# Kernel optimization log

Measured on AMD Instinct MI355X. Metric: run time of the kernel, lower is better.

Reference implementation:

```python
import jax, jax.numpy as jnp
import numpy as np

TEMPERATURE = 0.1
EPS = 1e-8


def setup_inputs() -> dict:
    key = jax.random.key(0)
    k1, k2 = jax.random.split(key)
    N, D = 4096, 512
    features = jax.random.normal(k1, (N, D), dtype=jnp.float32)
    labels = jax.random.randint(k2, (N,), 0, 100, dtype=jnp.int64)
    return {"features": features, "labels": labels}


def reference(features, labels):
    # FFT along feature dim -> complex (N, D)
    cf = jnp.fft.fft(features)
    N = cf.shape[0]

    # All-pairs complex dot product expressed as a GEMM:
    # Re(sum_d u_d * conj(v_d)) for every (anchor, contrast) pair -> (N, N)
    dot_real = jnp.real(cf @ jnp.conj(cf).T)

    # L2 norm of complex vectors: sqrt(sum |cf|^2) -> (N,)
    norms = jnp.linalg.norm(cf, axis=-1)

    sim = dot_real / (norms[:, None] * norms[None, :])  # cosine sim (N, N)
    sim = sim / TEMPERATURE

    # Positive-pair mask (same label), excluding the diagonal (self)
    same_label = (labels[:, None] == labels[None, :]).astype(sim.dtype)
    logits_mask = 1.0 - jnp.eye(N, dtype=sim.dtype)
    mask = same_label * logits_mask

    # Faithful to the original: exp without max-subtraction (sim bounded by 1/tau)
    exp_logits = jnp.exp(sim) * logits_mask
    log_prob = sim - jnp.log(exp_logits.sum(axis=1, keepdims=True))

    mean_log_prob_pos = (mask * log_prob).sum(axis=1) / (mask.sum(axis=1) + EPS)
    return -mean_log_prob_pos.mean()
```

## Files before the change

### kernel.cpp

```cpp
#include <hip/hip_runtime.h>
#include <hip/hip_bf16.h>
#include <math.h>


#define NROWS 4096
#define DDIM  512
#define TW    64
#define NBG   (NROWS / TW)
#define NTRI  (NBG * (NBG + 1) / 2)
#define NGRP  (NROWS / 16)
#define NSTEP (DDIM / 32)

typedef __attribute__((ext_vector_type(8))) short  short8;
typedef __attribute__((ext_vector_type(4))) float  floatx4;

__device__ inline unsigned short f2bf(float x) {
    unsigned u = __float_as_uint(x);
    return (unsigned short)((u + 0x7FFFu + ((u >> 16) & 1u)) >> 16);
}

__device__ inline float dpp_add16(float v) {
    v += __int_as_float(__builtin_amdgcn_update_dpp(
        0, __float_as_int(v), 0xB1, 0xF, 0xF, true));
    v += __int_as_float(__builtin_amdgcn_update_dpp(
        0, __float_as_int(v), 0x4E, 0xF, 0xF, true));
    v += __int_as_float(__builtin_amdgcn_update_dpp(
        0, __float_as_int(v), 0x141, 0xF, 0xF, true));
    v += __int_as_float(__builtin_amdgcn_update_dpp(
        0, __float_as_int(v), 0x140, 0xF, 0xF, true));
    return v;
}

__global__ __launch_bounds__(256) void prep_kernel(
    const float* __restrict__ F, const int* __restrict__ labels,
    unsigned short* __restrict__ Fbf, float* __restrict__ invn,
    float* __restrict__ S, float* __restrict__ P, int* __restrict__ hist) {
    const int g = blockIdx.x;
    const int t = threadIdx.x;
    const int l = t & 63;
    const int row = g * 16 + (l & 15);
    const int kbase = (l >> 4) * 8;
    short8* dst = (short8*)Fbf + (size_t)g * 1024 + t;
    float ss = 0.f;
#pragma unroll
    for (int c = 0; c < 4; ++c) {
        const int s = (t >> 6) + c * 4;
        const int k = s * 32 + kbase;
        const float4* src = (const float4*)(F + (size_t)row * DDIM + k);
        float4 v0 = src[0], v1 = src[1];
        ss += v0.x * v0.x + v0.y * v0.y + v0.z * v0.z + v0.w * v0.w
            + v1.x * v1.x + v1.y * v1.y + v1.z * v1.z + v1.w * v1.w;
        short8 o;
        o[0] = (short)f2bf(v0.x); o[1] = (short)f2bf(v0.y);
        o[2] = (short)f2bf(v0.z); o[3] = (short)f2bf(v0.w);
        o[4] = (short)f2bf(v1.x); o[5] = (short)f2bf(v1.y);
        o[6] = (short)f2bf(v1.z); o[7] = (short)f2bf(v1.w);
        dst[c * 256] = o;
    }
    ss += __shfl_xor(ss, 16, 64);
    ss += __shfl_xor(ss, 32, 64);
    __shared__ float red[4][16];
    if (l < 16) red[t >> 6][l] = ss;
    __syncthreads();
    if (t < 16) {
        float tot = red[0][t] + red[1][t] + red[2][t] + red[3][t];
        invn[g * 16 + t] = rsqrtf(tot) * 3.16227766017f;
        S[g * 16 + t] = 0.f;
        P[g * 16 + t] = 0.f;
    }
    if (g == 0) {
        __shared__ int h[128];
        if (t < 128) h[t] = 0;
        __syncthreads();
        for (int i = t; i < NROWS; i += 256) atomicAdd(&h[labels[i]], 1);
        __syncthreads();
        if (t < 128) hist[t] = h[t];
    }
}

__global__ __launch_bounds__(256) void fused_frag_kernel(
    const unsigned short* __restrict__ Fbf, const float* __restrict__ invn,
    const int* __restrict__ labels,
    float* __restrict__ S, float* __restrict__ P) {
    const int wid = blockIdx.x * 4 + (threadIdx.x >> 6);
    const int lane = threadIdx.x & 63;
    const int lrow = lane & 15;
    const int lquad = lane >> 4;

    int bi = (int)((129.0f - sqrtf(16641.0f - 8.0f * (float)wid)) * 0.5f);
    while (bi > 0 && bi * NBG - bi * (bi - 1) / 2 > wid) --bi;
    while ((bi + 1) * NBG - (bi + 1) * bi / 2 <= wid) ++bi;
    const int bj = bi + (wid - (bi * NBG - bi * (bi - 1) / 2));
    const bool diag = (bi == bj);
    const int ib = bi * TW, jb = bj * TW;

    const short8* FU = (const short8*)Fbf;
    const short8* pA = FU + (size_t)(bi * 4) * 1024 + lane;
    const short8* pB = FU + (size_t)(bj * 4) * 1024 + lane;

    floatx4 acc[4][4];
#pragma unroll
    for (int mi = 0; mi < 4; ++mi)
#pragma unroll
        for (int ni = 0; ni < 4; ++ni) acc[mi][ni] = (floatx4){0.f, 0.f, 0.f, 0.f};

    short8 af[3][4], bf[3][4];
#pragma unroll
    for (int p = 0; p < 2; ++p) {
#pragma unroll
        for (int mi = 0; mi < 4; ++mi) af[p][mi] = pA[mi * 1024 + p * 64];
#pragma unroll
        for (int ni = 0; ni < 4; ++ni) bf[p][ni] = pB[ni * 1024 + p * 64];
    }

#pragma unroll
    for (int ks = 0; ks < NSTEP; ++ks) {
        const int cur = ks % 3;
        if (ks + 2 < NSTEP) {
            const int nb = (ks + 2) % 3;
#pragma unroll
            for (int mi = 0; mi < 4; ++mi)
                af[nb][mi] = pA[mi * 1024 + (ks + 2) * 64];
#pragma unroll
            for (int ni = 0; ni < 4; ++ni)
                bf[nb][ni] = pB[ni * 1024 + (ks + 2) * 64];
        }
#pragma unroll
        for (int mi = 0; mi < 4; ++mi)
#pragma unroll
            for (int ni = 0; ni < 4; ++ni)
                acc[mi][ni] = __builtin_amdgcn_mfma_f32_16x16x32_bf16(
                    af[cur][mi], bf[cur][ni], acc[mi][ni], 0, 0, 0);
    }

    float inB[4];
    int lB[4];
#pragma unroll
    for (int ni = 0; ni < 4; ++ni) {
        int j = jb + ni * 16 + lrow;
        inB[ni] = invn[j];
        lB[ni] = labels[j];
    }
    float inA[4][4];
    int lA[4][4];
#pragma unroll
    for (int mi = 0; mi < 4; ++mi)
#pragma unroll
        for (int r = 0; r < 4; ++r) {
            int i = ib + mi * 16 + lquad * 4 + r;
            inA[mi][r] = invn[i];
            lA[mi][r] = labels[i];
        }

    float ecol[4] = {0.f, 0.f, 0.f, 0.f};
    float pcol[4] = {0.f, 0.f, 0.f, 0.f};

#pragma unroll
    for (int mi = 0; mi < 4; ++mi) {
#pragma unroll
        for (int r = 0; r < 4; ++r) {
            const int i = ib + mi * 16 + lquad * 4 + r;
            float es = 0.f, ps = 0.f;
#pragma unroll
            for (int ni = 0; ni < 4; ++ni) {
                const int j = jb + ni * 16 + lrow;
                float sim = acc[mi][ni][r] * inA[mi][r] * inB[ni];
                float e = __expf(sim);
                float pm = (lA[mi][r] == lB[ni]) ? sim : 0.f;
                if (diag && i == j) { e = 0.f; pm = 0.f; }
                es += e; ps += pm;
                ecol[ni] += e; pcol[ni] += pm;
            }
            es = dpp_add16(es);
            ps = dpp_add16(ps);
            if (lrow == 0) {
                atomicAdd(&S[i], es);
                atomicAdd(&P[i], ps);
            }
        }
    }

    if (!diag) {
#pragma unroll
        for (int ni = 0; ni < 4; ++ni) {
            float e = ecol[ni], pq = pcol[ni];
            e += __shfl_xor(e, 16, 64);
            e += __shfl_xor(e, 32, 64);
            pq += __shfl_xor(pq, 16, 64);
            pq += __shfl_xor(pq, 32, 64);
            if (lquad == 0) {
                int j = jb + ni * 16 + lrow;
                atomicAdd(&S[j], e);
                atomicAdd(&P[j], pq);
            }
        }
    }
}

__global__ __launch_bounds__(1024) void final_kernel(
    const float* __restrict__ S, const float* __restrict__ P,
    const int* __restrict__ labels, const int* __restrict__ hist,
    float* __restrict__ out) {
    float local = 0.f;
    for (int i = threadIdx.x; i < NROWS; i += 1024) {
        float cnt = (float)(hist[labels[i]] - 1);
        local += (P[i] - cnt * logf(S[i])) / (cnt + 1e-8f);
    }
#pragma unroll
    for (int m = 1; m < 64; m <<= 1) local += __shfl_xor(local, m, 64);
    __shared__ float red[16];
    int wave = threadIdx.x >> 6;
    if ((threadIdx.x & 63) == 0) red[wave] = local;
    __syncthreads();
    if (threadIdx.x == 0) {
        float s = 0.f;
#pragma unroll
        for (int w = 0; w < 16; ++w) s += red[w];
        out[0] = -s / (float)NROWS;
    }
}

extern "C" void kernel_launch(void* const* d_in, const int* in_sizes, int n_in,
                              void* d_out, int out_size, void* d_ws, size_t ws_size,
                              hipStream_t stream) {
    const float* F = (const float*)d_in[0];
    const int* labels = (const int*)d_in[1];
    float* out = (float*)d_out;

    unsigned short* Fbf = (unsigned short*)d_ws;
    float* invn = (float*)(Fbf + (size_t)NROWS * DDIM);
    float* S = invn + NROWS;
    float* P = S + NROWS;
    int* hist = (int*)(P + NROWS);

    prep_kernel<<<dim3(NGRP), dim3(256), 0, stream>>>(
        F, labels, Fbf, invn, S, P, hist);
    fused_frag_kernel<<<dim3(NTRI / 4), dim3(256), 0, stream>>>(
        Fbf, invn, labels, S, P);
    final_kernel<<<dim3(1), dim3(1024), 0, stream>>>(S, P, labels, hist, out);
}
```

Before: 94.62 us.

## Switch Gram GEMM to FP8 MFMA with LDS-staged 128-row bands

Features are quantized to FP8 instead of bf16 and the all-pairs Gram matrix now uses fp8 MFMA instructions, which halves operand bytes and doubles math rate. Each block now owns a 128x128 tile pair. The A band is staged into LDS via global_load_lds, while B fragments stream from global memory in a two-slot ring. Row and column partial sums are reduced in shared memory before one global atomic per row, which cuts global atomic traffic. FP8 precision may change the loss noticeably, and the exp of sims up to 10 amplifies those errors.

```diff
diff --git a/kernel.cpp b/kernel.cpp
--- a/kernel.cpp
+++ b/kernel.cpp
@@ -5,18 +5,21 @@
 
 #define NROWS 4096
 #define DDIM  512
-#define TW    64
-#define NBG   (NROWS / TW)
-#define NTRI  (NBG * (NBG + 1) / 2)
-#define NGRP  (NROWS / 16)
-#define NSTEP (DDIM / 32)
-
-typedef __attribute__((ext_vector_type(8))) short  short8;
-typedef __attribute__((ext_vector_type(4))) float  floatx4;
-
-__device__ inline unsigned short f2bf(float x) {
-    unsigned u = __float_as_uint(x);
-    return (unsigned short)((u + 0x7FFFu + ((u >> 16) & 1u)) >> 16);
+#define BAND  128
+#define NBAND (NROWS / BAND)
+#define NPAIR (NBAND * (NBAND + 1) / 2)
+#define NSTEP 16
+
+typedef __attribute__((ext_vector_type(4))) float floatx4;
+
+__device__ inline long f8pack(float v0, float v1, float v2, float v3,
+                              float v4, float v5, float v6, float v7) {
+    int lo = 0, hi = 0;
+    lo = __builtin_amdgcn_cvt_pk_fp8_f32(v0, v1, lo, false);
+    lo = __builtin_amdgcn_cvt_pk_fp8_f32(v2, v3, lo, true);
+    hi = __builtin_amdgcn_cvt_pk_fp8_f32(v4, v5, hi, false);
+    hi = __builtin_amdgcn_cvt_pk_fp8_f32(v6, v7, hi, true);
+    return ((long)(unsigned)lo) | ((long)hi << 32);
 }
 
 __device__ inline float dpp_add16(float v) {
@@ -33,40 +36,35 @@
 
 __global__ __launch_bounds__(256) void prep_kernel(
     const float* __restrict__ F, const int* __restrict__ labels,
-    unsigned short* __restrict__ Fbf, float* __restrict__ invn,
+    long* __restrict__ Fq, float* __restrict__ invn,
     float* __restrict__ S, float* __restrict__ P, int* __restrict__ hist) {
-    const int g = blockIdx.x;
-    const int t = threadIdx.x;
-    const int l = t & 63;
+    const int g = blockIdx.x, t = threadIdx.x;
+    const int l = t & 63, w = t >> 6;
     const int row = g * 16 + (l & 15);
-    const int kbase = (l >> 4) * 8;
-    short8* dst = (short8*)Fbf + (size_t)g * 1024 + t;
+    const int koff = ((l >> 4) & 3) * 8;
     float ss = 0.f;
 #pragma unroll
     for (int c = 0; c < 4; ++c) {
-        const int s = (t >> 6) + c * 4;
-        const int k = s * 32 + kbase;
+        const int s = c * 4 + w;
+        const int k = s * 32 + koff;
         const float4* src = (const float4*)(F + (size_t)row * DDIM + k);
-        float4 v0 = src[0], v1 = src[1];
-        ss += v0.x * v0.x + v0.y * v0.y + v0.z * v0.z + v0.w * v0.w
-            + v1.x * v1.x + v1.y * v1.y + v1.z * v1.z + v1.w * v1.w;
-        short8 o;
-        o[0] = (short)f2bf(v0.x); o[1] = (short)f2bf(v0.y);
-        o[2] = (short)f2bf(v0.z); o[3] = (short)f2bf(v0.w);
-        o[4] = (short)f2bf(v1.x); o[5] = (short)f2bf(v1.y);
-        o[6] = (short)f2bf(v1.z); o[7] = (short)f2bf(v1.w);
-        dst[c * 256] = o;
+        float4 a = src[0], b = src[1];
+        ss += a.x * a.x + a.y * a.y + a.z * a.z + a.w * a.w
+            + b.x * b.x + b.y * b.y + b.z * b.z + b.w * b.w;
+        Fq[(size_t)(g * 16 + s) * 64 + l] =
+            f8pack(a.x, a.y, a.z, a.w, b.x, b.y, b.z, b.w);
     }
     ss += __shfl_xor(ss, 16, 64);
     ss += __shfl_xor(ss, 32, 64);
-    __shared__ float red[4][16];
-    if (l < 16) red[t >> 6][l] = ss;
+    __shared__ float rs[4][16];
+    if (l < 16) rs[w][l] = ss;
     __syncthreads();
     if (t < 16) {
-        float tot = red[0][t] + red[1][t] + red[2][t] + red[3][t];
-        invn[g * 16 + t] = rsqrtf(tot) * 3.16227766017f;
-        S[g * 16 + t] = 0.f;
-        P[g * 16 + t] = 0.f;
+        float tot = rs[0][t] + rs[1][t] + rs[2][t] + rs[3][t];
+        int r = g * 16 + t;
+        invn[r] = rsqrtf(tot) * 3.16227766017f;
+        S[r] = 0.f;
+        P[r] = 0.f;
     }
     if (g == 0) {
         __shared__ int h[128];
@@ -78,95 +76,108 @@
     }
 }
 
-__global__ __launch_bounds__(256) void fused_frag_kernel(
-    const unsigned short* __restrict__ Fbf, const float* __restrict__ invn,
+__global__ __launch_bounds__(256) void gemm_kernel(
+    const long* __restrict__ Fq, const float* __restrict__ invn,
     const int* __restrict__ labels,
     float* __restrict__ S, float* __restrict__ P) {
-    const int wid = blockIdx.x * 4 + (threadIdx.x >> 6);
-    const int lane = threadIdx.x & 63;
-    const int lrow = lane & 15;
-    const int lquad = lane >> 4;
-
-    int bi = (int)((129.0f - sqrtf(16641.0f - 8.0f * (float)wid)) * 0.5f);
-    while (bi > 0 && bi * NBG - bi * (bi - 1) / 2 > wid) --bi;
-    while ((bi + 1) * NBG - (bi + 1) * bi / 2 <= wid) ++bi;
-    const int bj = bi + (wid - (bi * NBG - bi * (bi - 1) / 2));
+    __shared__ long Asl[BAND * 64];
+
+    const int tid = threadIdx.x;
+    const int w = tid >> 6, lane = tid & 63;
+    const int lrow = lane & 15, lquad = lane >> 4;
+
+    int wid = blockIdx.x;
+    int bi = 0;
+    while ((bi + 1) * NBAND - (bi + 1) * bi / 2 <= wid) ++bi;
+    const int bj = bi + (wid - (bi * NBAND - bi * (bi - 1) / 2));
     const bool diag = (bi == bj);
-    const int ib = bi * TW, jb = bj * TW;
-
-    const short8* FU = (const short8*)Fbf;
-    const short8* pA = FU + (size_t)(bi * 4) * 1024 + lane;
-    const short8* pB = FU + (size_t)(bj * 4) * 1024 + lane;
-
-    floatx4 acc[4][4];
-#pragma unroll
-    for (int mi = 0; mi < 4; ++mi)
-#pragma unroll
-        for (int ni = 0; ni < 4; ++ni) acc[mi][ni] = (floatx4){0.f, 0.f, 0.f, 0.f};
-
-    short8 af[3][4], bf[3][4];
-#pragma unroll
-    for (int p = 0; p < 2; ++p) {
-#pragma unroll
-        for (int mi = 0; mi < 4; ++mi) af[p][mi] = pA[mi * 1024 + p * 64];
-#pragma unroll
-        for (int ni = 0; ni < 4; ++ni) bf[p][ni] = pB[ni * 1024 + p * 64];
-    }
+    const int ib = bi * BAND, jb = bj * BAND;
+
+    {
+        const long* src = Fq + (size_t)bi * 8192;
+#pragma unroll
+        for (int r = 0; r < 16; ++r) {
+            __builtin_amdgcn_global_load_lds(
+                (const __attribute__((address_space(1))) unsigned int*)
+                    (src + r * 512 + (size_t)tid * 2),
+                (__attribute__((address_space(3))) unsigned int*)
+                    (Asl + r * 512 + tid * 2),
+                16, 0, 0);
+        }
+    }
+    __syncthreads();
+
+    floatx4 acc[8][2];
+#pragma unroll
+    for (int mi = 0; mi < 8; ++mi) {
+        acc[mi][0] = (floatx4){0.f, 0.f, 0.f, 0.f};
+        acc[mi][1] = (floatx4){0.f, 0.f, 0.f, 0.f};
+    }
+
+    const long* pB0 = Fq + (size_t)(bj * 8 + w * 2) * 1024 + lane;
+    const long* pB1 = Fq + (size_t)(bj * 8 + w * 2 + 1) * 1024 + lane;
+
+    long bring[2][2];
+    bring[0][0] = pB0[0];
+    bring[0][1] = pB1[0];
+    bring[1][0] = pB0[64];
+    bring[1][1] = pB1[64];
 
 #pragma unroll
     for (int ks = 0; ks < NSTEP; ++ks) {
-        const int cur = ks % 3;
+        const int cur = ks & 1;
+        const long b0 = bring[cur][0], b1 = bring[cur][1];
         if (ks + 2 < NSTEP) {
-            const int nb = (ks + 2) % 3;
-#pragma unroll
-            for (int mi = 0; mi < 4; ++mi)
-                af[nb][mi] = pA[mi * 1024 + (ks + 2) * 64];
-#pragma unroll
-            for (int ni = 0; ni < 4; ++ni)
-                bf[nb][ni] = pB[ni * 1024 + (ks + 2) * 64];
-        }
-#pragma unroll
-        for (int mi = 0; mi < 4; ++mi)
-#pragma unroll
-            for (int ni = 0; ni < 4; ++ni)
-                acc[mi][ni] = __builtin_amdgcn_mfma_f32_16x16x32_bf16(
-                    af[cur][mi], bf[cur][ni], acc[mi][ni], 0, 0, 0);
-    }
-
-    float inB[4];
-    int lB[4];
-#pragma unroll
-    for (int ni = 0; ni < 4; ++ni) {
-        int j = jb + ni * 16 + lrow;
+            bring[cur][0] = pB0[(ks + 2) * 64];
+            bring[cur][1] = pB1[(ks + 2) * 64];
+        }
+        long a[8];
+#pragma unroll
+        for (int mi = 0; mi < 8; ++mi)
+            a[mi] = Asl[(mi * 16 + ks) * 64 + lane];
+#pragma unroll
+        for (int mi = 0; mi < 8; ++mi) {
+            acc[mi][0] = __builtin_amdgcn_mfma_f32_16x16x32_fp8_fp8(
+                a[mi], b0, acc[mi][0], 0, 0, 0);
+            acc[mi][1] = __builtin_amdgcn_mfma_f32_16x16x32_fp8_fp8(
+                a[mi], b1, acc[mi][1], 0, 0, 0);
+        }
+    }
+
+    __syncthreads();
+    float* er = (float*)Asl;
+    float* pr = er + 128;
+    float* ec = pr + 128;
+    float* pc = ec + 128;
+    ((float*)Asl)[tid] = 0.f;
+    ((float*)Asl)[tid + 256] = 0.f;
+    __syncthreads();
+
+    float inB[2];
+    int lB[2];
+#pragma unroll
+    for (int ni = 0; ni < 2; ++ni) {
+        int j = jb + (w * 2 + ni) * 16 + lrow;
         inB[ni] = invn[j];
         lB[ni] = labels[j];
     }
-    float inA[4][4];
-    int lA[4][4];
-#pragma unroll
-    for (int mi = 0; mi < 4; ++mi)
+
+    float ecol[2] = {0.f, 0.f}, pcol[2] = {0.f, 0.f};
+#pragma unroll
+    for (int mi = 0; mi < 8; ++mi) {
 #pragma unroll
         for (int r = 0; r < 4; ++r) {
-            int i = ib + mi * 16 + lquad * 4 + r;
-            inA[mi][r] = invn[i];
-            lA[mi][r] = labels[i];
-        }
-
-    float ecol[4] = {0.f, 0.f, 0.f, 0.f};
-    float pcol[4] = {0.f, 0.f, 0.f, 0.f};
-
-#pragma unroll
-    for (int mi = 0; mi < 4; ++mi) {
-#pragma unroll
-        for (int r = 0; r < 4; ++r) {
-            const int i = ib + mi * 16 + lquad * 4 + r;
+            const int il = mi * 16 + lquad * 4 + r;
+            const int i = ib + il;
+            const float inA = invn[i];
+            const int lA = labels[i];
             float es = 0.f, ps = 0.f;
 #pragma unroll
-            for (int ni = 0; ni < 4; ++ni) {
-                const int j = jb + ni * 16 + lrow;
-                float sim = acc[mi][ni][r] * inA[mi][r] * inB[ni];
+            for (int ni = 0; ni < 2; ++ni) {
+                const int j = jb + (w * 2 + ni) * 16 + lrow;
+                float sim = acc[mi][ni][r] * inA * inB[ni];
                 float e = __expf(sim);
-                float pm = (lA[mi][r] == lB[ni]) ? sim : 0.f;
+                float pm = (lA == lB[ni]) ? sim : 0.f;
                 if (diag && i == j) { e = 0.f; pm = 0.f; }
                 es += e; ps += pm;
                 ecol[ni] += e; pcol[ni] += pm;
@@ -174,50 +185,50 @@
             es = dpp_add16(es);
             ps = dpp_add16(ps);
             if (lrow == 0) {
-                atomicAdd(&S[i], es);
-                atomicAdd(&P[i], ps);
+                atomicAdd(&er[il], es);
+                atomicAdd(&pr[il], ps);
             }
         }
     }
-
-    if (!diag) {
-#pragma unroll
-        for (int ni = 0; ni < 4; ++ni) {
-            float e = ecol[ni], pq = pcol[ni];
-            e += __shfl_xor(e, 16, 64);
-            e += __shfl_xor(e, 32, 64);
-            pq += __shfl_xor(pq, 16, 64);
-            pq += __shfl_xor(pq, 32, 64);
-            if (lquad == 0) {
-                int j = jb + ni * 16 + lrow;
-                atomicAdd(&S[j], e);
-                atomicAdd(&P[j], pq);
-            }
-        }
-    }
-}
-
-__global__ __launch_bounds__(1024) void final_kernel(
+#pragma unroll
+    for (int ni = 0; ni < 2; ++ni) {
+        float e = ecol[ni], p = pcol[ni];
+        e += __shfl_xor(e, 16, 64);
+        e += __shfl_xor(e, 32, 64);
+        p += __shfl_xor(p, 16, 64);
+        p += __shfl_xor(p, 32, 64);
+        if (lquad == 0) {
+            atomicAdd(&ec[(w * 2 + ni) * 16 + lrow], e);
+            atomicAdd(&pc[(w * 2 + ni) * 16 + lrow], p);
+        }
+    }
+    __syncthreads();
+    if (tid < 128) {
+        atomicAdd(&S[ib + tid], er[tid]);
+        atomicAdd(&P[ib + tid], pr[tid]);
+    } else if (!diag) {
+        atomicAdd(&S[jb + tid - 128], ec[tid - 128]);
+        atomicAdd(&P[jb + tid - 128], pc[tid - 128]);
+    }
+}
+
+__global__ __launch_bounds__(256) void final_kernel(
     const float* __restrict__ S, const float* __restrict__ P,
     const int* __restrict__ labels, const int* __restrict__ hist,
     float* __restrict__ out) {
     float local = 0.f;
-    for (int i = threadIdx.x; i < NROWS; i += 1024) {
+    for (int i = threadIdx.x; i < NROWS; i += 256) {
         float cnt = (float)(hist[labels[i]] - 1);
         local += (P[i] - cnt * logf(S[i])) / (cnt + 1e-8f);
     }
 #pragma unroll
     for (int m = 1; m < 64; m <<= 1) local += __shfl_xor(local, m, 64);
-    __shared__ float red[16];
+    __shared__ float red[4];
     int wave = threadIdx.x >> 6;
     if ((threadIdx.x & 63) == 0) red[wave] = local;
     __syncthreads();
-    if (threadIdx.x == 0) {
-        float s = 0.f;
-#pragma unroll
-        for (int w = 0; w < 16; ++w) s += red[w];
-        out[0] = -s / (float)NROWS;
-    }
+    if (threadIdx.x == 0)
+        out[0] = -(red[0] + red[1] + red[2] + red[3]) / (float)NROWS;
 }
 
 extern "C" void kernel_launch(void* const* d_in, const int* in_sizes, int n_in,
@@ -227,15 +238,15 @@
     const int* labels = (const int*)d_in[1];
     float* out = (float*)d_out;
 
-    unsigned short* Fbf = (unsigned short*)d_ws;
-    float* invn = (float*)(Fbf + (size_t)NROWS * DDIM);
+    long* Fq = (long*)d_ws;
+    float* invn = (float*)((char*)d_ws + (size_t)NROWS * DDIM);
     float* S = invn + NROWS;
     float* P = S + NROWS;
     int* hist = (int*)(P + NROWS);
 
-    prep_kernel<<<dim3(NGRP), dim3(256), 0, stream>>>(
-        F, labels, Fbf, invn, S, P, hist);
-    fused_frag_kernel<<<dim3(NTRI / 4), dim3(256), 0, stream>>>(
-        Fbf, invn, labels, S, P);
-    final_kernel<<<dim3(1), dim3(1024), 0, stream>>>(S, P, labels, hist, out);
-}
+    prep_kernel<<<dim3(NROWS / 16), dim3(256), 0, stream>>>(
+        F, labels, Fq, invn, S, P, hist);
+    gemm_kernel<<<dim3(NPAIR), dim3(256), 0, stream>>>(
+        Fq, invn, labels, S, P);
+    final_kernel<<<dim3(1), dim3(256), 0, stream>>>(S, P, labels, hist, out);
+}
```

New measurement: 95.06 us. Within noise of the previous version (+0.5%).
